# Kernel tuning notes

Measured on AMD Instinct MI355X. Metric: run time of the kernel, lower is better.

Reference implementation:

```python
import jax, jax.numpy as jnp
import numpy as np
from jax import lax

N = 20000; E = 640000
D_IN = 64; F1 = 256; H = 256
HEADS = 8; HC = 128; DH = HC // HEADS
NA = 8; MS = 64


def setup_inputs() -> dict:
    key = jax.random.key(0)
    ks = jax.random.split(key, 40)
    def w(k, shape, fan):
        return (jax.random.normal(k, shape, jnp.float32) / np.sqrt(fan)).astype(jnp.float32)
    inp = {}
    inp['state'] = jax.random.normal(ks[0], (N, D_IN), jnp.float32)
    inp['message'] = jax.random.normal(ks[1], (N, MS), jnp.float32)
    inp['edge_index'] = jax.random.randint(ks[2], (2, E), 0, N)
    # fc1 / fc2
    inp['W_fc1'] = w(ks[3], (D_IN, F1), D_IN); inp['b_fc1'] = jnp.zeros((F1,), jnp.float32)
    inp['W_fc2'] = w(ks[4], (MS, F1), MS);    inp['b_fc2'] = jnp.zeros((F1,), jnp.float32)
    # GRU: 2 layers, torch layout W_ih [3H, in], W_hh [3H, H]
    inp['Wih0'] = w(ks[5], (3 * H, F1), F1); inp['Whh0'] = w(ks[6], (3 * H, H), H)
    inp['bih0'] = jnp.zeros((3 * H,), jnp.float32); inp['bhh0'] = jnp.zeros((3 * H,), jnp.float32)
    inp['Wih1'] = w(ks[7], (3 * H, H), H); inp['Whh1'] = w(ks[8], (3 * H, H), H)
    inp['bih1'] = jnp.zeros((3 * H,), jnp.float32); inp['bhh1'] = jnp.zeros((3 * H,), jnp.float32)
    # GAT layer 1: in H -> HEADS heads of DH (concat -> HC)
    inp['Wg1'] = w(ks[9], (H, HC), H)
    inp['as1'] = w(ks[10], (HEADS, DH), DH); inp['ad1'] = w(ks[11], (HEADS, DH), DH)
    inp['bg1'] = jnp.zeros((HC,), jnp.float32)
    # GAT layer 2: HC -> HC
    inp['Wg2'] = w(ks[12], (HC, HC), HC)
    inp['as2'] = w(ks[13], (HEADS, DH), DH); inp['ad2'] = w(ks[14], (HEADS, DH), DH)
    inp['bg2'] = jnp.zeros((HC,), jnp.float32)
    # heads
    inp['Wc'] = w(ks[15], (HC, 1), HC); inp['bc'] = jnp.zeros((1,), jnp.float32)
    inp['Wmu'] = w(ks[16], (HC + H, NA), HC + H); inp['bmu'] = jnp.zeros((NA,), jnp.float32)
    inp['Wm'] = w(ks[17], (HC, MS), HC); inp['bm'] = jnp.zeros((MS,), jnp.float32)
    return inp


def gru_layer(x_seq, Wih, Whh, bih, bhh):
    # x_seq: [N, in]; torch GRUCell math, batch size 1 squeezed
    h_dim = Whh.shape[1]
    def step(h, x):
        gi = x @ Wih.T + bih
        gh = h @ Whh.T + bhh
        ir, iz, inn = jnp.split(gi, 3)
        hr, hz, hn = jnp.split(gh, 3)
        r = jax.nn.sigmoid(ir + hr)
        z = jax.nn.sigmoid(iz + hz)
        n = jnp.tanh(inn + r * hn)
        h_new = (1.0 - z) * n + z * h
        return h_new, h_new
    h0 = jnp.zeros((h_dim,), x_seq.dtype)
    _, ys = lax.scan(step, h0, x_seq)
    return ys  # [N, h_dim]


def gat_conv(x, W, a_src, a_dst, b, src, dst):
    # x: [N, in] -> [N, HEADS*DH], edge softmax over incoming edges per dst node
    n = x.shape[0]
    h = (x @ W).reshape(n, HEADS, DH)
    e_src = jnp.einsum('nhd,hd->nh', h, a_src)  # [N, HEADS]
    e_dst = jnp.einsum('nhd,hd->nh', h, a_dst)
    e = jax.nn.leaky_relu(e_src[src] + e_dst[dst], 0.2)  # [E, HEADS]
    emax = jax.ops.segment_max(e, dst, num_segments=n)
    emax = lax.stop_gradient(jnp.where(jnp.isfinite(emax), emax, 0.0))
    p = jnp.exp(e - emax[dst])
    denom = jax.ops.segment_sum(p, dst, num_segments=n)
    alpha = p / (denom[dst] + 1e-16)  # [E, HEADS]
    msgs = h[src] * alpha[:, :, None]  # [E, HEADS, DH]
    out = jax.ops.segment_sum(msgs, dst, num_segments=n)
    return out.reshape(n, HEADS * DH) + b


def reference(state, message, edge_index, W_fc1, b_fc1, W_fc2, b_fc2,
              Wih0, Whh0, bih0, bhh0, Wih1, Whh1, bih1, bhh1,
              Wg1, as1, ad1, bg1, Wg2, as2, ad2, bg2,
              Wc, bc, Wmu, bmu, Wm, bm):
    src, dst = edge_index[0], edge_index[1]
    x = jax.nn.relu(state @ W_fc1 + b_fc1)          # [N, F1]
    m = jax.nn.relu(message @ W_fc2 + b_fc2)        # [N, F1]
    x = x + m
    x = gru_layer(x, Wih0, Whh0, bih0, bhh0)        # [N, H]
    x = gru_layer(x, Wih1, Whh1, bih1, bhh1)
    x = jax.nn.relu(x)
    xg = gat_conv(x, Wg1, as1, ad1, bg1, src, dst)  # [N, HC]
    xg = jax.nn.relu(xg)
    xg = gat_conv(xg, Wg2, as2, ad2, bg2, src, dst)
    comm = jax.nn.sigmoid(xg @ Wc + bc)             # [N, 1]
    mu = jnp.tanh(jnp.concatenate([x, xg], axis=-1) @ Wmu + bmu)  # [N, NA]
    msg_out = jnp.tanh(xg @ Wm + bm)                # [N, MS]
    return comm, msg_out, mu
```

## Files before the change

### kernel.cpp

```cpp
#include <hip/hip_runtime.h>
#include <stdint.h>

#define N_NODES 20000
#define E_EDGES 640000
#define F1 256
#define HDIM 256
#define G3 768
#define HEADS 8
#define HC 128
#define DH 16
#define NA 8
#define MS 64

typedef _Float16 h2 __attribute__((ext_vector_type(2)));

__device__ __forceinline__ float fdot2(uint32_t a, uint32_t b, float c) {
#if __has_builtin(__builtin_amdgcn_fdot2)
  return __builtin_amdgcn_fdot2(__builtin_bit_cast(h2, a), __builtin_bit_cast(h2, b), c, false);
#else
  h2 x = __builtin_bit_cast(h2, a), y = __builtin_bit_cast(h2, b);
  return c + (float)x[0] * (float)y[0] + (float)x[1] * (float)y[1];
#endif
}

__device__ __forceinline__ float fexp2(float x) { return __builtin_amdgcn_exp2f(x); }
__device__ __forceinline__ float frcp(float x)  { return __builtin_amdgcn_rcpf(x); }
__device__ __forceinline__ float sigm(float x)  { return frcp(1.f + fexp2(-1.44269504f * x)); }
__device__ __forceinline__ float tanh_(float x) {
  x = fminf(20.f, fmaxf(-20.f, x));
  float t = fexp2(2.88539008f * x);
  return (t - 1.f) * frcp(t + 1.f);
}
__device__ __forceinline__ float leaky(float x) { return (x > 0.f) ? x : 0.2f * x; }
__device__ __forceinline__ unsigned fenc(float f) {
  unsigned u = __float_as_uint(f);
  return (u & 0x80000000u) ? ~u : (u | 0x80000000u);
}
__device__ __forceinline__ float fdec(unsigned u) {
  return __uint_as_float((u & 0x80000000u) ? (u ^ 0x80000000u) : ~u);
}

#define GF_BIAS 1
#define GF_RELU_OUT 2
#define GF_ACC 4
#define GF_RELU_A 8
#define GF_BT 16

template <int FLAGS>
__global__ __launch_bounds__(256) void gemm_k(const float* __restrict__ A,
                                              const float* __restrict__ B,
                                              const float* __restrict__ bias,
                                              float* __restrict__ C,
                                              int M, int K, int P) {
  __shared__ float As[64][68];
  __shared__ float Bs[64][68];
  int colTiles = P >> 6;
  int bx = blockIdx.x % colTiles;
  int by = blockIdx.x / colTiles;
  int row0 = by * 64, col0 = bx * 64;
  int tid = threadIdx.x;
  int tx = tid & 15, ty = tid >> 4;
  float acc[4][4] = {};
  for (int k0 = 0; k0 < K; k0 += 64) {
    {
      int r = tid >> 2, kq = (tid & 3) * 16;
      int gr = row0 + r;
      const float* ap = A + (size_t)gr * K + k0 + kq;
#pragma unroll
      for (int j = 0; j < 4; j++) {
        float4 v = make_float4(0.f, 0.f, 0.f, 0.f);
        if (gr < M) v = *(const float4*)(ap + 4 * j);
        if (FLAGS & GF_RELU_A) {
          v.x = fmaxf(v.x, 0.f); v.y = fmaxf(v.y, 0.f);
          v.z = fmaxf(v.z, 0.f); v.w = fmaxf(v.w, 0.f);
        }
        As[kq + 4 * j + 0][r] = v.x; As[kq + 4 * j + 1][r] = v.y;
        As[kq + 4 * j + 2][r] = v.z; As[kq + 4 * j + 3][r] = v.w;
      }
    }
    if (FLAGS & GF_BT) {
      int n = tid >> 2, kq = (tid & 3) * 16;
      const float* bp = B + (size_t)(col0 + n) * K + k0 + kq;
#pragma unroll
      for (int j = 0; j < 4; j++) {
        float4 v = *(const float4*)(bp + 4 * j);
        Bs[kq + 4 * j + 0][n] = v.x; Bs[kq + 4 * j + 1][n] = v.y;
        Bs[kq + 4 * j + 2][n] = v.z; Bs[kq + 4 * j + 3][n] = v.w;
      }
    } else {
      int kk = tid >> 2, nq = (tid & 3) * 16;
      const float* bp = B + (size_t)(k0 + kk) * P + col0 + nq;
#pragma unroll
      for (int j = 0; j < 4; j++)
        *(float4*)&Bs[kk][nq + 4 * j] = *(const float4*)(bp + 4 * j);
    }
    __syncthreads();
#pragma unroll
    for (int kk = 0; kk < 64; kk++) {
      float4 av = *(const float4*)&As[kk][ty * 4];
      float4 bv = *(const float4*)&Bs[kk][tx * 4];
      float a4[4] = {av.x, av.y, av.z, av.w};
      float b4[4] = {bv.x, bv.y, bv.z, bv.w};
#pragma unroll
      for (int i = 0; i < 4; i++)
#pragma unroll
        for (int j = 0; j < 4; j++) acc[i][j] = fmaf(a4[i], b4[j], acc[i][j]);
    }
    __syncthreads();
  }
#pragma unroll
  for (int i = 0; i < 4; i++) {
    int gr = row0 + ty * 4 + i;
    if (gr >= M) continue;
#pragma unroll
    for (int j = 0; j < 4; j++) {
      int gc = col0 + tx * 4 + j;
      float v = acc[i][j];
      if (FLAGS & GF_BIAS) v += bias[gc];
      if (FLAGS & GF_RELU_OUT) v = fmaxf(v, 0.f);
      size_t o = (size_t)gr * P + gc;
      if (FLAGS & GF_ACC) C[o] += v; else C[o] = v;
    }
  }
}

__global__ __launch_bounds__(256) void prep_w(const float* __restrict__ Whh,
                                              uint32_t* __restrict__ Wpk) {
  int idx = blockIdx.x * 256 + threadIdx.x;
  if (idx >= 192 * 512) return;
  int q = idx >> 9, t = idx & 511;
  int g = t >> 2, c = t & 3;
  int a = q >> 5, p = q & 31;
  int row = (a % 3) * 256 + 2 * g + (a / 3);
  int k = 64 * c + 2 * p;
  h2 v = { (_Float16)Whh[row * 256 + k], (_Float16)Whh[row * 256 + k + 1] };
  Wpk[idx] = __builtin_bit_cast(uint32_t, v);
}

__global__ __launch_bounds__(512, 2) void gru_scan(const float* __restrict__ GI,
                                                   const uint32_t* __restrict__ Wpk,
                                                   const float* __restrict__ bhh,
                                                   float* __restrict__ Hout) {
  __shared__ __align__(16) uint32_t hb[2][4][36];
  int tid = threadIdx.x;
  int g = tid >> 2, c = tid & 3;
  int lane = tid & 63;
  uint32_t w[192];
#pragma unroll
  for (int q = 0; q < 192; q++) w[q] = Wpk[q * 512 + tid];
  for (int i = tid; i < 2 * 4 * 36; i += 512) ((uint32_t*)hb)[i] = 0;
  bool gatel = ((c & 1) == 0);
  int j = 2 * g + (c >> 1);
  float bh_r = 0, bh_z = 0, bh_n = 0, hreg = 0, gr = 0, gz = 0, gn = 0;
  if (gatel) {
    bh_r = bhh[j]; bh_z = bhh[256 + j]; bh_n = bhh[512 + j];
    gr = GI[j]; gz = GI[256 + j]; gn = GI[512 + j];
  }
  __syncthreads();
  int buf = 0;
  const int bl = lane & ~3;
#pragma unroll 1
  for (int t = 0; t < N_NODES; t++) {
    float pgr = 0, pgz = 0, pgn = 0;
    if (gatel) {
      int tn = (t + 1 < N_NODES) ? t + 1 : t;
      const float* gp = GI + (size_t)tn * G3;
      pgr = gp[j]; pgz = gp[256 + j]; pgn = gp[512 + j];
    }
    float a0 = 0, a1 = 0, a2 = 0, a3 = 0, a4 = 0, a5 = 0;
    const uint32_t* hc = &hb[buf][c][0];
    uint4 A0 = *(const uint4*)(hc + 0);
    uint4 B0 = *(const uint4*)(hc + 4);
#pragma unroll
    for (int qq = 0; qq < 4; qq++) {
      uint4 A1 = A0, B1 = B0;
      if (qq < 3) {
        A1 = *(const uint4*)(hc + 8 * (qq + 1));
        B1 = *(const uint4*)(hc + 8 * (qq + 1) + 4);
      }
      uint32_t hp[8] = {A0.x, A0.y, A0.z, A0.w, B0.x, B0.y, B0.z, B0.w};
#pragma unroll
      for (int pp = 0; pp < 8; pp++) {
        int p = 8 * qq + pp;
        a0 = fdot2(w[0 * 32 + p], hp[pp], a0);
        a1 = fdot2(w[1 * 32 + p], hp[pp], a1);
        a2 = fdot2(w[2 * 32 + p], hp[pp], a2);
        a3 = fdot2(w[3 * 32 + p], hp[pp], a3);
        a4 = fdot2(w[4 * 32 + p], hp[pp], a4);
        a5 = fdot2(w[5 * 32 + p], hp[pp], a5);
      }
      A0 = A1; B0 = B1;
    }
    float v6 = 0.f, v7 = 0.f;
    float u0, u1, u2, u3;
    {
      float t0 = __shfl_xor(a0, 2, 64), t4 = __shfl_xor(a4, 2, 64);
      u0 = (c & 2) ? a4 + t4 : a0 + t0;
      float t1 = __shfl_xor(a1, 2, 64), t5 = __shfl_xor(a5, 2, 64);
      u1 = (c & 2) ? a5 + t5 : a1 + t1;
      float t2 = __shfl_xor(a2, 2, 64), t6 = __shfl_xor(v6, 2, 64);
      u2 = (c & 2) ? v6 + t6 : a2 + t2;
      float t3 = __shfl_xor(a3, 2, 64), t7 = __shfl_xor(v7, 2, 64);
      u3 = (c & 2) ? v7 + t7 : a3 + t3;
    }
    float f0, f1;
    {
      float t0 = __shfl_xor(u0, 1, 64), t2 = __shfl_xor(u2, 1, 64);
      f0 = (c & 1) ? u2 + t2 : u0 + t0;
      float t1 = __shfl_xor(u1, 1, 64), t3 = __shfl_xor(u3, 1, 64);
      f1 = (c & 1) ? u3 + t3 : u1 + t1;
    }
    float ta = __shfl(f0, bl + 1, 64);
    float tb = __shfl(f1, bl + 1, 64);
    if (gatel) {
      float Sr = (c == 0) ? f0 : tb;
      float Sz = (c == 0) ? f1 : f0;
      float Sn = (c == 0) ? ta : f1;
      float r = sigm(gr + bh_r + Sr);
      float z = sigm(gz + bh_z + Sz);
      float n = tanh_(gn + r * (Sn + bh_n));
      float hn = (1.f - z) * n + z * hreg;
      hreg = hn;
      Hout[(size_t)t * HDIM + j] = hn;
      int pj = j >> 1, cc = pj >> 5, half = j & 1;
      ushort* hw = (ushort*)&hb[buf ^ 1][cc][0];
      hw[(pj & 31) * 2 + half] = __builtin_bit_cast(uint16_t, (_Float16)hn);
      gr = pgr; gz = pgz; gn = pgn;
    }
    __syncthreads();
    buf ^= 1;
  }
}

__global__ __launch_bounds__(256) void esed_k(const float* __restrict__ Hg,
                                              const float* __restrict__ a_s,
                                              const float* __restrict__ a_d,
                                              float* __restrict__ es, float* __restrict__ ed) {
  int idx = blockIdx.x * 256 + threadIdx.x;
  if (idx >= N_NODES * HEADS) return;
  int n = idx >> 3, hd = idx & 7;
  const float* hp = Hg + (size_t)n * HC + hd * DH;
  float s = 0, d = 0;
#pragma unroll
  for (int i = 0; i < DH; i++) {
    float h = hp[i];
    s = fmaf(h, a_s[hd * DH + i], s);
    d = fmaf(h, a_d[hd * DH + i], d);
  }
  es[idx] = s; ed[idx] = d;
}

__global__ __launch_bounds__(256) void esmax_k(const float* __restrict__ es,
                                               unsigned* __restrict__ m) {
  int idx = blockIdx.x * 256 + threadIdx.x;
  float v = (idx < N_NODES * HEADS) ? es[idx] : -1e30f;
#pragma unroll
  for (int mask = 32; mask >= 8; mask >>= 1) v = fmaxf(v, __shfl_xor(v, mask, 64));
  if ((threadIdx.x & 63) < 8) atomicMax(&m[threadIdx.x & 7], fenc(v));
}

__global__ __launch_bounds__(256) void attA_k(const int* __restrict__ ei,
                                              const float* __restrict__ es,
                                              const float* __restrict__ ed,
                                              const unsigned* __restrict__ esm,
                                              float* __restrict__ den) {
  int idx = blockIdx.x * 256 + threadIdx.x;
  if (idx >= E_EDGES * HEADS) return;
  int e = idx >> 3, hd = idx & 7;
  int s = ei[e], d = ei[E_EDGES + e];
  float edv = ed[d * 8 + hd];
  float lv = leaky(es[s * 8 + hd] + edv);
  float cb = leaky(fdec(esm[hd]) + edv);
  float p = fexp2(1.44269504f * (lv - cb));
  atomicAdd(&den[d * 8 + hd], p);
}

__global__ __launch_bounds__(256) void attB_k(const int* __restrict__ ei,
                                              const float* __restrict__ es,
                                              const float* __restrict__ ed,
                                              const unsigned* __restrict__ esm,
                                              const float* __restrict__ den,
                                              const float* __restrict__ Hg,
                                              float* __restrict__ outb) {
  int idx = blockIdx.x * 256 + threadIdx.x;
  if (idx >= E_EDGES * HEADS) return;
  int e = idx >> 3, hd = idx & 7;
  int s = ei[e], d = ei[E_EDGES + e];
  float edv = ed[d * 8 + hd];
  float lv = leaky(es[s * 8 + hd] + edv);
  float cb = leaky(fdec(esm[hd]) + edv);
  float p = fexp2(1.44269504f * (lv - cb));
  float alpha = p * frcp(den[d * 8 + hd] + 1e-16f);
  const float4* hp = (const float4*)(Hg + (size_t)s * HC + hd * DH);
  float* op = outb + (size_t)d * HC + hd * DH;
#pragma unroll
  for (int q = 0; q < 4; q++) {
    float4 h4 = hp[q];
    atomicAdd(op + 4 * q + 0, alpha * h4.x);
    atomicAdd(op + 4 * q + 1, alpha * h4.y);
    atomicAdd(op + 4 * q + 2, alpha * h4.z);
    atomicAdd(op + 4 * q + 3, alpha * h4.w);
  }
}

__global__ __launch_bounds__(256) void biasrelu_k(const float* __restrict__ in,
                                                  const float* __restrict__ b,
                                                  float* __restrict__ o) {
  int idx = blockIdx.x * 256 + threadIdx.x;
  if (idx >= N_NODES * HC) return;
  o[idx] = fmaxf(in[idx] + b[idx & (HC - 1)], 0.f);
}

__global__ __launch_bounds__(64) void heads_k(const float* __restrict__ xgb,
                                              const float* __restrict__ bg2,
                                              const float* __restrict__ H2,
                                              const float* __restrict__ Wc, const float* __restrict__ bc,
                                              const float* __restrict__ Wmu, const float* __restrict__ bmu,
                                              const float* __restrict__ Wm, const float* __restrict__ bm,
                                              float* __restrict__ out) {
  int n = blockIdx.x, l = threadIdx.x;
  __shared__ float xg[HC];
  __shared__ float xr[HDIM];
  for (int i = l; i < HC; i += 64) xg[i] = xgb[(size_t)n * HC + i] + bg2[i];
  for (int i = l; i < HDIM; i += 64) xr[i] = fmaxf(H2[(size_t)n * HDIM + i], 0.f);
  __syncthreads();
  float acc = bm[l];
#pragma unroll 8
  for (int k = 0; k < HC; k++) acc = fmaf(xg[k], Wm[k * MS + l], acc);
  out[N_NODES + (size_t)n * MS + l] = tanh_(acc);
  if (l < NA) {
    float a = bmu[l];
    for (int k = 0; k < HDIM; k++) a = fmaf(xr[k], Wmu[k * NA + l], a);
    for (int k = 0; k < HC; k++) a = fmaf(xg[k], Wmu[(HDIM + k) * NA + l], a);
    out[N_NODES + (size_t)N_NODES * MS + (size_t)n * NA + l] = tanh_(a);
  }
  if (l == 0) {
    float a = bc[0];
    for (int k = 0; k < HC; k++) a = fmaf(xg[k], Wc[k], a);
    out[n] = sigm(a);
  }
}

extern "C" void kernel_launch(void* const* d_in, const int* in_sizes, int n_in,
                              void* d_out, int out_size, void* d_ws, size_t ws_size,
                              hipStream_t stream) {
  const float* state = (const float*)d_in[0];
  const float* message = (const float*)d_in[1];
  const int* ei = (const int*)d_in[2];
  const float* Wfc1 = (const float*)d_in[3]; const float* bfc1 = (const float*)d_in[4];
  const float* Wfc2 = (const float*)d_in[5]; const float* bfc2 = (const float*)d_in[6];
  const float* Wih0 = (const float*)d_in[7]; const float* Whh0 = (const float*)d_in[8];
  const float* bih0 = (const float*)d_in[9]; const float* bhh0 = (const float*)d_in[10];
  const float* Wih1 = (const float*)d_in[11]; const float* Whh1 = (const float*)d_in[12];
  const float* bih1 = (const float*)d_in[13]; const float* bhh1 = (const float*)d_in[14];
  const float* Wg1 = (const float*)d_in[15]; const float* as1 = (const float*)d_in[16];
  const float* ad1 = (const float*)d_in[17]; const float* bg1 = (const float*)d_in[18];
  const float* Wg2 = (const float*)d_in[19]; const float* as2 = (const float*)d_in[20];
  const float* ad2 = (const float*)d_in[21]; const float* bg2 = (const float*)d_in[22];
  const float* Wc = (const float*)d_in[23]; const float* bc = (const float*)d_in[24];
  const float* Wmu = (const float*)d_in[25]; const float* bmu = (const float*)d_in[26];
  const float* Wm = (const float*)d_in[27]; const float* bm = (const float*)d_in[28];

  float* ws = (float*)d_ws;
  float* GI = ws;
  float* HGa = ws;
  float* HGb = ws + 2560000;
  float* X2  = ws + 5120000;
  float* ES  = ws + 7680000;
  float* ED  = ws + 7840000;
  float* DEN = ws + 8000000;
  unsigned* ESM = (unsigned*)(ws + 8160000);
  float* X  = ws + 15360000;
  float* H2 = ws + 20480000;
  uint32_t* Wpk = (uint32_t*)(ws + 25600000);
  float* out = (float*)d_out;

  int rt = (N_NODES + 63) / 64;

  gemm_k<GF_BIAS | GF_RELU_OUT><<<rt * 4, 256, 0, stream>>>(state, Wfc1, bfc1, X, N_NODES, 64, 256);
  gemm_k<GF_BIAS | GF_RELU_OUT | GF_ACC><<<rt * 4, 256, 0, stream>>>(message, Wfc2, bfc2, X, N_NODES, 64, 256);
  gemm_k<GF_BIAS | GF_BT><<<rt * 12, 256, 0, stream>>>(X, Wih0, bih0, GI, N_NODES, 256, G3);
  prep_w<<<384, 256, 0, stream>>>(Whh0, Wpk);
  gru_scan<<<1, 512, 0, stream>>>(GI, Wpk, bhh0, X);
  gemm_k<GF_BIAS | GF_BT><<<rt * 12, 256, 0, stream>>>(X, Wih1, bih1, GI, N_NODES, 256, G3);
  prep_w<<<384, 256, 0, stream>>>(Whh1, Wpk);
  gru_scan<<<1, 512, 0, stream>>>(GI, Wpk, bhh1, H2);
  gemm_k<GF_RELU_A><<<rt * 2, 256, 0, stream>>>(H2, Wg1, nullptr, HGa, N_NODES, 256, HC);
  esed_k<<<625, 256, 0, stream>>>(HGa, as1, ad1, ES, ED);
  hipMemsetAsync(DEN, 0, 160000 * 4, stream);
  hipMemsetAsync(ESM, 0, 8 * 4, stream);
  esmax_k<<<625, 256, 0, stream>>>(ES, ESM);
  attA_k<<<20000, 256, 0, stream>>>(ei, ES, ED, ESM, DEN);
  hipMemsetAsync(HGb, 0, (size_t)2560000 * 4, stream);
  attB_k<<<20000, 256, 0, stream>>>(ei, ES, ED, ESM, DEN, HGa, HGb);
  biasrelu_k<<<10000, 256, 0, stream>>>(HGb, bg1, X2);
  gemm_k<0><<<rt * 2, 256, 0, stream>>>(X2, Wg2, nullptr, HGa, N_NODES, HC, HC);
  esed_k<<<625, 256, 0, stream>>>(HGa, as2, ad2, ES, ED);
  hipMemsetAsync(DEN, 0, 160000 * 4, stream);
  hipMemsetAsync(ESM, 0, 8 * 4, stream);
  esmax_k<<<625, 256, 0, stream>>>(ES, ESM);
  attA_k<<<20000, 256, 0, stream>>>(ei, ES, ED, ESM, DEN);
  hipMemsetAsync(HGb, 0, (size_t)2560000 * 4, stream);
  attB_k<<<20000, 256, 0, stream>>>(ei, ES, ED, ESM, DEN, HGa, HGb);
  heads_k<<<N_NODES, 64, 0, stream>>>(HGb, bg2, H2, Wc, bc, Wmu, bmu, Wm, bm, out);
}
```

Before: 64.69 ms.

## Replace atomic edge-scatter GAT with CSR gather and vectorize GRU weight registers

```diff
diff --git a/kernel.cpp b/kernel.cpp
--- a/kernel.cpp
+++ b/kernel.cpp
@@ -127,8 +127,11 @@
 __global__ __launch_bounds__(256) void prep_w(const float* __restrict__ Whh,
                                               uint32_t* __restrict__ Wpk) {
   int idx = blockIdx.x * 256 + threadIdx.x;
-  if (idx >= 192 * 512) return;
-  int q = idx >> 9, t = idx & 511;
+  if (idx >= 48 * 2048) return;
+  int i = idx >> 11;
+  int rem = idx & 2047;
+  int t = rem >> 2, comp = rem & 3;
+  int q = 4 * i + comp;
   int g = t >> 2, c = t & 3;
   int a = q >> 5, p = q & 31;
   int row = (a % 3) * 256 + 2 * g + (a / 3);
@@ -136,6 +139,14 @@
   h2 v = { (_Float16)Whh[row * 256 + k], (_Float16)Whh[row * 256 + k + 1] };
   Wpk[idx] = __builtin_bit_cast(uint32_t, v);
 }
+
+#define WD(i) uint4 W##i = Wp4[(i) * 512 + tid];
+#define DOT6(A,B,C,D,E,F, m, hv) \
+  a0 = fdot2(A.m, hv, a0); a1 = fdot2(B.m, hv, a1); a2 = fdot2(C.m, hv, a2); \
+  a3 = fdot2(D.m, hv, a3); a4 = fdot2(E.m, hv, a4); a5 = fdot2(F.m, hv, a5);
+#define DOT4(H, A,B,C,D,E,F) \
+  DOT6(A,B,C,D,E,F, x, H.x) DOT6(A,B,C,D,E,F, y, H.y) \
+  DOT6(A,B,C,D,E,F, z, H.z) DOT6(A,B,C,D,E,F, w, H.w)
 
 __global__ __launch_bounds__(512, 2) void gru_scan(const float* __restrict__ GI,
                                                    const uint32_t* __restrict__ Wpk,
@@ -145,9 +156,13 @@
   int tid = threadIdx.x;
   int g = tid >> 2, c = tid & 3;
   int lane = tid & 63;
-  uint32_t w[192];
-#pragma unroll
-  for (int q = 0; q < 192; q++) w[q] = Wpk[q * 512 + tid];
+  const uint4* Wp4 = (const uint4*)Wpk;
+  WD(0)  WD(1)  WD(2)  WD(3)  WD(4)  WD(5)  WD(6)  WD(7)
+  WD(8)  WD(9)  WD(10) WD(11) WD(12) WD(13) WD(14) WD(15)
+  WD(16) WD(17) WD(18) WD(19) WD(20) WD(21) WD(22) WD(23)
+  WD(24) WD(25) WD(26) WD(27) WD(28) WD(29) WD(30) WD(31)
+  WD(32) WD(33) WD(34) WD(35) WD(36) WD(37) WD(38) WD(39)
+  WD(40) WD(41) WD(42) WD(43) WD(44) WD(45) WD(46) WD(47)
   for (int i = tid; i < 2 * 4 * 36; i += 512) ((uint32_t*)hb)[i] = 0;
   bool gatel = ((c & 1) == 0);
   int j = 2 * g + (c >> 1);
@@ -168,29 +183,17 @@
       pgr = gp[j]; pgz = gp[256 + j]; pgn = gp[512 + j];
     }
     float a0 = 0, a1 = 0, a2 = 0, a3 = 0, a4 = 0, a5 = 0;
-    const uint32_t* hc = &hb[buf][c][0];
-    uint4 A0 = *(const uint4*)(hc + 0);
-    uint4 B0 = *(const uint4*)(hc + 4);
-#pragma unroll
-    for (int qq = 0; qq < 4; qq++) {
-      uint4 A1 = A0, B1 = B0;
-      if (qq < 3) {
-        A1 = *(const uint4*)(hc + 8 * (qq + 1));
-        B1 = *(const uint4*)(hc + 8 * (qq + 1) + 4);
-      }
-      uint32_t hp[8] = {A0.x, A0.y, A0.z, A0.w, B0.x, B0.y, B0.z, B0.w};
-#pragma unroll
-      for (int pp = 0; pp < 8; pp++) {
-        int p = 8 * qq + pp;
-        a0 = fdot2(w[0 * 32 + p], hp[pp], a0);
-        a1 = fdot2(w[1 * 32 + p], hp[pp], a1);
-        a2 = fdot2(w[2 * 32 + p], hp[pp], a2);
-        a3 = fdot2(w[3 * 32 + p], hp[pp], a3);
-        a4 = fdot2(w[4 * 32 + p], hp[pp], a4);
-        a5 = fdot2(w[5 * 32 + p], hp[pp], a5);
-      }
-      A0 = A1; B0 = B1;
-    }
+    const uint4* hc4 = (const uint4*)(&hb[buf][c][0]);
+    uint4 Ha = hc4[0];
+    uint4 Hb = hc4[1];
+    DOT4(Ha, W0, W8,  W16, W24, W32, W40)  Ha = hc4[2];
+    DOT4(Hb, W1, W9,  W17, W25, W33, W41)  Hb = hc4[3];
+    DOT4(Ha, W2, W10, W18, W26, W34, W42)  Ha = hc4[4];
+    DOT4(Hb, W3, W11, W19, W27, W35, W43)  Hb = hc4[5];
+    DOT4(Ha, W4, W12, W20, W28, W36, W44)  Ha = hc4[6];
+    DOT4(Hb, W5, W13, W21, W29, W37, W45)  Hb = hc4[7];
+    DOT4(Ha, W6, W14, W22, W30, W38, W46)
+    DOT4(Hb, W7, W15, W23, W31, W39, W47)
     float v6 = 0.f, v7 = 0.f;
     float u0, u1, u2, u3;
     {
@@ -259,56 +262,96 @@
   if ((threadIdx.x & 63) < 8) atomicMax(&m[threadIdx.x & 7], fenc(v));
 }
 
-__global__ __launch_bounds__(256) void attA_k(const int* __restrict__ ei,
-                                              const float* __restrict__ es,
-                                              const float* __restrict__ ed,
-                                              const unsigned* __restrict__ esm,
-                                              float* __restrict__ den) {
-  int idx = blockIdx.x * 256 + threadIdx.x;
-  if (idx >= E_EDGES * HEADS) return;
-  int e = idx >> 3, hd = idx & 7;
-  int s = ei[e], d = ei[E_EDGES + e];
-  float edv = ed[d * 8 + hd];
-  float lv = leaky(es[s * 8 + hd] + edv);
-  float cb = leaky(fdec(esm[hd]) + edv);
-  float p = fexp2(1.44269504f * (lv - cb));
-  atomicAdd(&den[d * 8 + hd], p);
-}
-
-__global__ __launch_bounds__(256) void attB_k(const int* __restrict__ ei,
-                                              const float* __restrict__ es,
-                                              const float* __restrict__ ed,
-                                              const unsigned* __restrict__ esm,
-                                              const float* __restrict__ den,
-                                              const float* __restrict__ Hg,
-                                              float* __restrict__ outb) {
-  int idx = blockIdx.x * 256 + threadIdx.x;
-  if (idx >= E_EDGES * HEADS) return;
-  int e = idx >> 3, hd = idx & 7;
-  int s = ei[e], d = ei[E_EDGES + e];
-  float edv = ed[d * 8 + hd];
-  float lv = leaky(es[s * 8 + hd] + edv);
-  float cb = leaky(fdec(esm[hd]) + edv);
-  float p = fexp2(1.44269504f * (lv - cb));
-  float alpha = p * frcp(den[d * 8 + hd] + 1e-16f);
-  const float4* hp = (const float4*)(Hg + (size_t)s * HC + hd * DH);
-  float* op = outb + (size_t)d * HC + hd * DH;
-#pragma unroll
-  for (int q = 0; q < 4; q++) {
-    float4 h4 = hp[q];
-    atomicAdd(op + 4 * q + 0, alpha * h4.x);
-    atomicAdd(op + 4 * q + 1, alpha * h4.y);
-    atomicAdd(op + 4 * q + 2, alpha * h4.z);
-    atomicAdd(op + 4 * q + 3, alpha * h4.w);
-  }
-}
-
-__global__ __launch_bounds__(256) void biasrelu_k(const float* __restrict__ in,
-                                                  const float* __restrict__ b,
-                                                  float* __restrict__ o) {
-  int idx = blockIdx.x * 256 + threadIdx.x;
-  if (idx >= N_NODES * HC) return;
-  o[idx] = fmaxf(in[idx] + b[idx & (HC - 1)], 0.f);
+__global__ __launch_bounds__(256) void deg_k(const int* __restrict__ ei, int* __restrict__ deg) {
+  int e = blockIdx.x * 256 + threadIdx.x;
+  if (e >= E_EDGES) return;
+  atomicAdd(&deg[ei[E_EDGES + e]], 1);
+}
+
+__global__ __launch_bounds__(1024) void scan_k(const int* __restrict__ deg, int* __restrict__ off) {
+  __shared__ int wsum[16];
+  __shared__ int carry;
+  int tid = threadIdx.x, lane = tid & 63, wv = tid >> 6;
+  if (tid == 0) carry = 0;
+  __syncthreads();
+  for (int base = 0; base < N_NODES; base += 1024) {
+    int i = base + tid;
+    int v = (i < N_NODES) ? deg[i] : 0;
+    int s = v;
+#pragma unroll
+    for (int d = 1; d < 64; d <<= 1) {
+      int t = __shfl_up(s, d, 64);
+      if (lane >= d) s += t;
+    }
+    if (lane == 63) wsum[wv] = s;
+    __syncthreads();
+    if (wv == 0 && lane < 16) {
+      int t = wsum[lane];
+#pragma unroll
+      for (int d = 1; d < 16; d <<= 1) {
+        int u = __shfl_up(t, d, 64);
+        if (lane >= d) t += u;
+      }
+      wsum[lane] = t;
+    }
+    __syncthreads();
+    int prev = (wv > 0) ? wsum[wv - 1] : 0;
+    int excl = carry + prev + s - v;
+    if (i < N_NODES) off[i] = excl;
+    int total = wsum[15];
+    __syncthreads();
+    if (tid == 0) carry += total;
+    __syncthreads();
+  }
+  if (tid == 0) off[N_NODES] = carry;
+}
+
+__global__ __launch_bounds__(256) void scatter_k(const int* __restrict__ ei,
+                                                 const int* __restrict__ off,
+                                                 int* __restrict__ cnt,
+                                                 int* __restrict__ csr_src) {
+  int e = blockIdx.x * 256 + threadIdx.x;
+  if (e >= E_EDGES) return;
+  int d = ei[E_EDGES + e];
+  int pos = off[d] + atomicAdd(&cnt[d], 1);
+  csr_src[pos] = ei[e];
+}
+
+template <int RELU>
+__global__ __launch_bounds__(256) void gather_k(const int* __restrict__ off,
+                                                const int* __restrict__ csr_src,
+                                                const float* __restrict__ es,
+                                                const float* __restrict__ ed,
+                                                const unsigned* __restrict__ esm,
+                                                const float* __restrict__ Hg,
+                                                const float* __restrict__ bias,
+                                                float* __restrict__ out) {
+  int wv = threadIdx.x >> 6, lane = threadIdx.x & 63;
+  int d = blockIdx.x * 4 + wv;
+  if (d >= N_NODES) return;
+  int hd0 = lane >> 4, hd1 = 4 + (lane >> 4);
+  float ed0 = ed[d * 8 + hd0], ed1 = ed[d * 8 + hd1];
+  float cb0 = leaky(fdec(esm[hd0]) + ed0);
+  float cb1 = leaky(fdec(esm[hd1]) + ed1);
+  int e0 = off[d], e1 = off[d + 1];
+  float acc0 = 0, acc1 = 0, den0 = 0, den1 = 0;
+  for (int i = e0; i < e1; i++) {
+    int s = csr_src[i];
+    float p0 = fexp2(1.44269504f * (leaky(es[s * 8 + hd0] + ed0) - cb0));
+    float p1 = fexp2(1.44269504f * (leaky(es[s * 8 + hd1] + ed1) - cb1));
+    float h0 = Hg[(size_t)s * HC + lane];
+    float h1 = Hg[(size_t)s * HC + 64 + lane];
+    acc0 = fmaf(p0, h0, acc0); acc1 = fmaf(p1, h1, acc1);
+    den0 += p0; den1 += p1;
+  }
+  float o0 = acc0 * frcp(den0 + 1e-16f);
+  float o1 = acc1 * frcp(den1 + 1e-16f);
+  if (RELU) {
+    o0 = fmaxf(o0 + bias[lane], 0.f);
+    o1 = fmaxf(o1 + bias[64 + lane], 0.f);
+  }
+  out[(size_t)d * HC + lane] = o0;
+  out[(size_t)d * HC + 64 + lane] = o1;
 }
 
 __global__ __launch_bounds__(64) void heads_k(const float* __restrict__ xgb,
@@ -368,8 +411,11 @@
   float* X2  = ws + 5120000;
   float* ES  = ws + 7680000;
   float* ED  = ws + 7840000;
-  float* DEN = ws + 8000000;
   unsigned* ESM = (unsigned*)(ws + 8160000);
+  int* DEG = (int*)(ws + 8200000);
+  int* OFF = (int*)(ws + 8230000);
+  int* CNT = (int*)(ws + 8260000);
+  int* CSR = (int*)(ws + 8300000);
   float* X  = ws + 15360000;
   float* H2 = ws + 20480000;
   uint32_t* Wpk = (uint32_t*)(ws + 25600000);
@@ -385,22 +431,20 @@
   gemm_k<GF_BIAS | GF_BT><<<rt * 12, 256, 0, stream>>>(X, Wih1, bih1, GI, N_NODES, 256, G3);
   prep_w<<<384, 256, 0, stream>>>(Whh1, Wpk);
   gru_scan<<<1, 512, 0, stream>>>(GI, Wpk, bhh1, H2);
+  hipMemsetAsync(DEG, 0, N_NODES * 4, stream);
+  hipMemsetAsync(CNT, 0, N_NODES * 4, stream);
+  deg_k<<<2500, 256, 0, stream>>>(ei, DEG);
+  scan_k<<<1, 1024, 0, stream>>>(DEG, OFF);
+  scatter_k<<<2500, 256, 0, stream>>>(ei, OFF, CNT, CSR);
   gemm_k<GF_RELU_A><<<rt * 2, 256, 0, stream>>>(H2, Wg1, nullptr, HGa, N_NODES, 256, HC);
   esed_k<<<625, 256, 0, stream>>>(HGa, as1, ad1, ES, ED);
-  hipMemsetAsync(DEN, 0, 160000 * 4, stream);
   hipMemsetAsync(ESM, 0, 8 * 4, stream);
   esmax_k<<<625, 256, 0, stream>>>(ES, ESM);
-  attA_k<<<20000, 256, 0, stream>>>(ei, ES, ED, ESM, DEN);
-  hipMemsetAsync(HGb, 0, (size_t)2560000 * 4, stream);
-  attB_k<<<20000, 256, 0, stream>>>(ei, ES, ED, ESM, DEN, HGa, HGb);
-  biasrelu_k<<<10000, 256, 0, stream>>>(HGb, bg1, X2);
+  gather_k<1><<<5000, 256, 0, stream>>>(OFF, CSR, ES, ED, ESM, HGa, bg1, X2);
   gemm_k<0><<<rt * 2, 256, 0, stream>>>(X2, Wg2, nullptr, HGa, N_NODES, HC, HC);
   esed_k<<<625, 256, 0, stream>>>(HGa, as2, ad2, ES, ED);
-  hipMemsetAsync(DEN, 0, 160000 * 4, stream);
   hipMemsetAsync(ESM, 0, 8 * 4, stream);
   esmax_k<<<625, 256, 0, stream>>>(ES, ESM);
-  attA_k<<<20000, 256, 0, stream>>>(ei, ES, ED, ESM, DEN);
-  hipMemsetAsync(HGb, 0, (size_t)2560000 * 4, stream);
-  attB_k<<<20000, 256, 0, stream>>>(ei, ES, ED, ESM, DEN, HGa, HGb);
+  gather_k<0><<<5000, 256, 0, stream>>>(OFF, CSR, ES, ED, ESM, HGa, nullptr, HGb);
   heads_k<<<N_NODES, 64, 0, stream>>>(HGb, bg2, H2, Wc, bc, Wmu, bmu, Wm, bm, out);
 }
```

After: 58.39 ms. 1.11x faster.
